# Kernel tuning notes

Hardware: AMD Instinct MI355X
Metric: run time of the kernel (lower is better)

The kernel has to match this reference:

```python
import jax, jax.numpy as jnp
import numpy as np

B, IN, OUT, K = 512, 65536, 16384, 32

def setup_inputs() -> dict:
    key = jax.random.key(0)
    k1, k2, k3 = jax.random.split(key, 3)
    x = jax.random.normal(k1, (B, IN), dtype=jnp.float32)
    indices = jax.random.randint(k2, (OUT, K), 0, IN, dtype=jnp.int32)
    weight = jax.random.normal(k3, (OUT, K), dtype=jnp.float32) * 0.1
    bias = jnp.zeros((OUT,), dtype=jnp.float32)
    return {"x": x, "indices": indices, "weight": weight, "bias": bias}

def reference(x, indices, weight, bias):
    # Gather per-output feature subsets: (B, OUT, K)
    x_sel = x[:, indices]
    # Weighted sum over K connections per output, plus bias: (B, OUT)
    out = jnp.einsum('bok,ok->bo', x_sel, weight) + bias
    return out
```

## Files before the change

### kernel.cpp

```cpp
#include <hip/hip_runtime.h>

#define B_DIM   512
#define IN_DIM  65536
#define OUT_DIM 16384
#define K_DIM   32

static __device__ __forceinline__ unsigned short f2bf(float f) {
    unsigned u = __builtin_bit_cast(unsigned, f);
    unsigned r = (u + 0x7FFFu + ((u >> 16) & 1u)) >> 16;
    return (unsigned short)r;
}

static __device__ __forceinline__ float fcomp(float4 v, int c) {
    switch (c & 3) { case 0: return v.x; case 1: return v.y; case 2: return v.z; default: return v.w; }
}

__global__ __launch_bounds__(512) void transpose_bf16_k(const float* __restrict__ x,
                                                        unsigned short* __restrict__ xT) {
    const int c0 = blockIdx.x * 32;
    const int b  = threadIdx.x;
    const float4* p = (const float4*)(x + (size_t)b * IN_DIM + c0);
    float4 v[8];
    #pragma unroll
    for (int j = 0; j < 8; ++j) v[j] = p[j];
    #pragma unroll
    for (int c = 0; c < 32; ++c) {
        xT[(size_t)(c0 + c) * B_DIM + b] = f2bf(fcomp(v[c >> 2], c));
    }
}

#define SE 520

__global__ __launch_bounds__(256, 4) void sparse_main(const unsigned short* __restrict__ xT,
                                                      const int*   __restrict__ idxp,
                                                      const float* __restrict__ wp,
                                                      const float* __restrict__ biasp,
                                                      float*       __restrict__ out) {
    __shared__ float lds[8][SE];
    const int o_blk = blockIdx.x * 8;
    const int t    = threadIdx.x;
    const int wid  = t >> 6;
    const int lane = t & 63;
    const int b8   = lane * 8;

    const int   iv = idxp[o_blk * K_DIM + wid * 64 + lane];
    const float wv = wp  [o_blk * K_DIM + wid * 64 + lane];

    float4 a0[2], a1[2];
    #pragma unroll
    for (int oo = 0; oo < 2; ++oo) {
        a0[oo] = make_float4(0.f, 0.f, 0.f, 0.f);
        a1[oo] = make_float4(0.f, 0.f, 0.f, 0.f);
    }

    #pragma unroll
    for (int oo = 0; oo < 2; ++oo) {
        #pragma unroll
        for (int k = 0; k < K_DIM; ++k) {
            const int L = oo * 32 + k;
            const int   sidx = __builtin_amdgcn_readlane(iv, L);
            const float sw   = __int_as_float(
                __builtin_amdgcn_readlane(__float_as_int(wv), L));
            const uint4 u = *(const uint4*)(xT + ((size_t)sidx << 9) + b8);
            a0[oo].x = fmaf(sw, __int_as_float(u.x << 16),          a0[oo].x);
            a0[oo].y = fmaf(sw, __int_as_float(u.x & 0xFFFF0000u),  a0[oo].y);
            a0[oo].z = fmaf(sw, __int_as_float(u.y << 16),          a0[oo].z);
            a0[oo].w = fmaf(sw, __int_as_float(u.y & 0xFFFF0000u),  a0[oo].w);
            a1[oo].x = fmaf(sw, __int_as_float(u.z << 16),          a1[oo].x);
            a1[oo].y = fmaf(sw, __int_as_float(u.z & 0xFFFF0000u),  a1[oo].y);
            a1[oo].z = fmaf(sw, __int_as_float(u.w << 16),          a1[oo].z);
            a1[oo].w = fmaf(sw, __int_as_float(u.w & 0xFFFF0000u),  a1[oo].w);
        }
    }

    #pragma unroll
    for (int oo = 0; oo < 2; ++oo) {
        const float bv = biasp[o_blk + wid * 2 + oo];
        a0[oo].x += bv; a0[oo].y += bv; a0[oo].z += bv; a0[oo].w += bv;
        a1[oo].x += bv; a1[oo].y += bv; a1[oo].z += bv; a1[oo].w += bv;
        *(float4*)(&lds[wid * 2 + oo][b8])     = a0[oo];
        *(float4*)(&lds[wid * 2 + oo][b8 + 4]) = a1[oo];
    }
    __syncthreads();

    #pragma unroll
    for (int p = 0; p < 4; ++p) {
        const int q = p * 1024 + t * 4;
        const int b = q >> 3;
        const int o = q & 7;
        float4 v;
        v.x = lds[o + 0][b];
        v.y = lds[o + 1][b];
        v.z = lds[o + 2][b];
        v.w = lds[o + 3][b];
        *(float4*)(out + (size_t)b * OUT_DIM + o_blk + o) = v;
    }
}

__global__ void sparse_fallback(const float* __restrict__ x,
                                const int*   __restrict__ idxp,
                                const float* __restrict__ wp,
                                const float* __restrict__ biasp,
                                float*       __restrict__ out) {
    const int i = blockIdx.x * blockDim.x + threadIdx.x;
    if (i >= B_DIM * OUT_DIM) return;
    const int b = i / OUT_DIM;
    const int o = i % OUT_DIM;
    float a = biasp[o];
    for (int k = 0; k < K_DIM; ++k) {
        const int idx = idxp[o * K_DIM + k];
        a = fmaf(wp[o * K_DIM + k], x[(size_t)b * IN_DIM + idx], a);
    }
    out[i] = a;
}

extern "C" void kernel_launch(void* const* d_in, const int* in_sizes, int n_in,
                              void* d_out, int out_size, void* d_ws, size_t ws_size,
                              hipStream_t stream) {
    const float* x       = (const float*)d_in[0];
    const int*   indices = (const int*)  d_in[1];
    const float* weight  = (const float*)d_in[2];
    const float* bias    = (const float*)d_in[3];
    float*       out     = (float*)d_out;

    const size_t need = (size_t)IN_DIM * B_DIM * sizeof(unsigned short);
    if (ws_size >= need) {
        unsigned short* xT = (unsigned short*)d_ws;
        transpose_bf16_k<<<IN_DIM / 32, 512, 0, stream>>>(x, xT);
        sparse_main<<<OUT_DIM / 8, 256, 0, stream>>>(xT, indices, weight, bias, out);
    } else {
        const int n = B_DIM * OUT_DIM;
        sparse_fallback<<<(n + 255) / 256, 256, 0, stream>>>(x, indices, weight, bias, out);
    }
}
```

Measured before the change: 351.5 us.

## Use one output per wave with 512 threads and software-pipelined gathers

Each block now runs 8 waves of 512 threads, one output feature per wave instead of two, which doubles the waves available to hide gather latency. The K loop is hand-unrolled into double-buffered batches of four 16-byte loads, so the next eight gathers are issued before the FMAs on the previous batch. This should raise memory-level parallelism on the random row gathers, at the cost of more live registers per thread and launch_bounds(512,4) pressure. The output transpose loop is adjusted to the wider block.

```diff
diff --git a/kernel.cpp b/kernel.cpp
--- a/kernel.cpp
+++ b/kernel.cpp
@@ -31,7 +31,7 @@
 
 #define SE 520
 
-__global__ __launch_bounds__(256, 4) void sparse_main(const unsigned short* __restrict__ xT,
+__global__ __launch_bounds__(512, 4) void sparse_main(const unsigned short* __restrict__ xT,
                                                       const int*   __restrict__ idxp,
                                                       const float* __restrict__ wp,
                                                       const float* __restrict__ biasp,
@@ -42,58 +42,74 @@
     const int wid  = t >> 6;
     const int lane = t & 63;
     const int b8   = lane * 8;
+    const int o    = o_blk + wid;
 
-    const int   iv = idxp[o_blk * K_DIM + wid * 64 + lane];
-    const float wv = wp  [o_blk * K_DIM + wid * 64 + lane];
+    const int   iv = idxp[o * K_DIM + (lane & 31)];
+    const float wv = wp  [o * K_DIM + (lane & 31)];
 
-    float4 a0[2], a1[2];
-    #pragma unroll
-    for (int oo = 0; oo < 2; ++oo) {
-        a0[oo] = make_float4(0.f, 0.f, 0.f, 0.f);
-        a1[oo] = make_float4(0.f, 0.f, 0.f, 0.f);
-    }
+    const unsigned short* base = xT + b8;
 
-    #pragma unroll
-    for (int oo = 0; oo < 2; ++oo) {
-        #pragma unroll
-        for (int k = 0; k < K_DIM; ++k) {
-            const int L = oo * 32 + k;
-            const int   sidx = __builtin_amdgcn_readlane(iv, L);
-            const float sw   = __int_as_float(
-                __builtin_amdgcn_readlane(__float_as_int(wv), L));
-            const uint4 u = *(const uint4*)(xT + ((size_t)sidx << 9) + b8);
-            a0[oo].x = fmaf(sw, __int_as_float(u.x << 16),          a0[oo].x);
-            a0[oo].y = fmaf(sw, __int_as_float(u.x & 0xFFFF0000u),  a0[oo].y);
-            a0[oo].z = fmaf(sw, __int_as_float(u.y << 16),          a0[oo].z);
-            a0[oo].w = fmaf(sw, __int_as_float(u.y & 0xFFFF0000u),  a0[oo].w);
-            a1[oo].x = fmaf(sw, __int_as_float(u.z << 16),          a1[oo].x);
-            a1[oo].y = fmaf(sw, __int_as_float(u.z & 0xFFFF0000u),  a1[oo].y);
-            a1[oo].z = fmaf(sw, __int_as_float(u.w << 16),          a1[oo].z);
-            a1[oo].w = fmaf(sw, __int_as_float(u.w & 0xFFFF0000u),  a1[oo].w);
-        }
-    }
+    float4 accL = make_float4(0.f, 0.f, 0.f, 0.f);
+    float4 accH = make_float4(0.f, 0.f, 0.f, 0.f);
 
-    #pragma unroll
-    for (int oo = 0; oo < 2; ++oo) {
-        const float bv = biasp[o_blk + wid * 2 + oo];
-        a0[oo].x += bv; a0[oo].y += bv; a0[oo].z += bv; a0[oo].w += bv;
-        a1[oo].x += bv; a1[oo].y += bv; a1[oo].z += bv; a1[oo].w += bv;
-        *(float4*)(&lds[wid * 2 + oo][b8])     = a0[oo];
-        *(float4*)(&lds[wid * 2 + oo][b8 + 4]) = a1[oo];
-    }
+    uint4 A0, A1, A2, A3, B0, B1, B2, B3;
+    float wA0, wA1, wA2, wA3, wB0, wB1, wB2, wB3;
+
+#define GLOAD(dst, wdst, kk) do { \
+        const int si_ = __builtin_amdgcn_readlane(iv, (kk)); \
+        wdst = __int_as_float(__builtin_amdgcn_readlane(__float_as_int(wv), (kk))); \
+        dst = *(const uint4*)(base + ((size_t)si_ << 9)); \
+    } while (0)
+
+#define FMA8(u, sw) do { \
+        accL.x = fmaf(sw, __int_as_float(u.x << 16),         accL.x); \
+        accL.y = fmaf(sw, __int_as_float(u.x & 0xFFFF0000u), accL.y); \
+        accL.z = fmaf(sw, __int_as_float(u.y << 16),         accL.z); \
+        accL.w = fmaf(sw, __int_as_float(u.y & 0xFFFF0000u), accL.w); \
+        accH.x = fmaf(sw, __int_as_float(u.z << 16),         accH.x); \
+        accH.y = fmaf(sw, __int_as_float(u.z & 0xFFFF0000u), accH.y); \
+        accH.z = fmaf(sw, __int_as_float(u.w << 16),         accH.z); \
+        accH.w = fmaf(sw, __int_as_float(u.w & 0xFFFF0000u), accH.w); \
+    } while (0)
+
+    GLOAD(A0, wA0,  0); GLOAD(A1, wA1,  1); GLOAD(A2, wA2,  2); GLOAD(A3, wA3,  3);
+    GLOAD(B0, wB0,  4); GLOAD(B1, wB1,  5); GLOAD(B2, wB2,  6); GLOAD(B3, wB3,  7);
+    FMA8(A0, wA0); FMA8(A1, wA1); FMA8(A2, wA2); FMA8(A3, wA3);
+    GLOAD(A0, wA0,  8); GLOAD(A1, wA1,  9); GLOAD(A2, wA2, 10); GLOAD(A3, wA3, 11);
+    FMA8(B0, wB0); FMA8(B1, wB1); FMA8(B2, wB2); FMA8(B3, wB3);
+    GLOAD(B0, wB0, 12); GLOAD(B1, wB1, 13); GLOAD(B2, wB2, 14); GLOAD(B3, wB3, 15);
+    FMA8(A0, wA0); FMA8(A1, wA1); FMA8(A2, wA2); FMA8(A3, wA3);
+    GLOAD(A0, wA0, 16); GLOAD(A1, wA1, 17); GLOAD(A2, wA2, 18); GLOAD(A3, wA3, 19);
+    FMA8(B0, wB0); FMA8(B1, wB1); FMA8(B2, wB2); FMA8(B3, wB3);
+    GLOAD(B0, wB0, 20); GLOAD(B1, wB1, 21); GLOAD(B2, wB2, 22); GLOAD(B3, wB3, 23);
+    FMA8(A0, wA0); FMA8(A1, wA1); FMA8(A2, wA2); FMA8(A3, wA3);
+    GLOAD(A0, wA0, 24); GLOAD(A1, wA1, 25); GLOAD(A2, wA2, 26); GLOAD(A3, wA3, 27);
+    FMA8(B0, wB0); FMA8(B1, wB1); FMA8(B2, wB2); FMA8(B3, wB3);
+    GLOAD(B0, wB0, 28); GLOAD(B1, wB1, 29); GLOAD(B2, wB2, 30); GLOAD(B3, wB3, 31);
+    FMA8(A0, wA0); FMA8(A1, wA1); FMA8(A2, wA2); FMA8(A3, wA3);
+    FMA8(B0, wB0); FMA8(B1, wB1); FMA8(B2, wB2); FMA8(B3, wB3);
+
+#undef GLOAD
+#undef FMA8
+
+    const float bv = biasp[o];
+    accL.x += bv; accL.y += bv; accL.z += bv; accL.w += bv;
+    accH.x += bv; accH.y += bv; accH.z += bv; accH.w += bv;
+    *(float4*)(&lds[wid][b8])     = accL;
+    *(float4*)(&lds[wid][b8 + 4]) = accH;
     __syncthreads();
 
     #pragma unroll
-    for (int p = 0; p < 4; ++p) {
-        const int q = p * 1024 + t * 4;
+    for (int p = 0; p < 2; ++p) {
+        const int q = p * 2048 + t * 4;
         const int b = q >> 3;
-        const int o = q & 7;
+        const int oo = q & 7;
         float4 v;
-        v.x = lds[o + 0][b];
-        v.y = lds[o + 1][b];
-        v.z = lds[o + 2][b];
-        v.w = lds[o + 3][b];
-        *(float4*)(out + (size_t)b * OUT_DIM + o_blk + o) = v;
+        v.x = lds[oo + 0][b];
+        v.y = lds[oo + 1][b];
+        v.z = lds[oo + 2][b];
+        v.w = lds[oo + 3][b];
+        *(float4*)(out + (size_t)b * OUT_DIM + o_blk + oo) = v;
     }
 }
 
@@ -127,7 +143,7 @@
     if (ws_size >= need) {
         unsigned short* xT = (unsigned short*)d_ws;
         transpose_bf16_k<<<IN_DIM / 32, 512, 0, stream>>>(x, xT);
-        sparse_main<<<OUT_DIM / 8, 256, 0, stream>>>(xT, indices, weight, bias, out);
+        sparse_main<<<OUT_DIM / 8, 512, 0, stream>>>(xT, indices, weight, bias, out);
     } else {
         const int n = B_DIM * OUT_DIM;
         sparse_fallback<<<(n + 255) / 256, 256, 0, stream>>>(x, indices, weight, bias, out);
```

New measurement: 311.7 us. -11.3%, faster.
